# Performance work log

Hardware: AMD Instinct MI355X
Metric: run time of the kernel (lower is better)

Reference implementation:

```python
import jax, jax.numpy as jnp
import numpy as np

N_NODES = 100000
N_EDGES = 3200000
NUM_CLASSES = 10
SQRT3 = 3.0 ** 0.5


def setup_inputs() -> dict:
    key = jax.random.key(0)
    ks = jax.random.split(key, 20)
    f32 = jnp.float32
    return {
        "positions": jax.random.normal(ks[0], (N_NODES, 3), f32) * 5.0,
        "edge_src": jax.random.randint(ks[1], (N_EDGES,), 0, N_NODES, jnp.int32),
        "edge_dst": jax.random.randint(ks[2], (N_EDGES,), 0, N_NODES, jnp.int32),
        # layer1: TP('1x0e', sh) -> '1x0e + 1x1o' -> Linear -> '5x0e + 5x1o'
        "W0_1": jax.random.normal(ks[3], (5, 1), f32),
        "W1_1": jax.random.normal(ks[4], (5, 1, 3), f32),
        "b_1": jax.random.normal(ks[5], (5,), f32),
        # gate1: Linear('5x0e+5x1o' -> '10x0e') uses only the 5 input 0e irreps
        "Wg1": jax.random.normal(ks[6], (10, 5), f32),
        "bg1": jax.random.normal(ks[7], (10,), f32),
        # layer2: TP('5x0e+5x1o', sh) -> 10x0e + 10x1o (+5x1e unused) -> '5x0e+5x1o'
        "W0_2": jax.random.normal(ks[8], (5, 10), f32),
        "W1_2": jax.random.normal(ks[9], (5, 10, 3), f32),
        "b_2": jax.random.normal(ks[10], (5,), f32),
        "Wg2": jax.random.normal(ks[11], (10, 5), f32),
        "bg2": jax.random.normal(ks[12], (10,), f32),
        # layer3: TP -> 10x0e used -> '5x0e'
        "W0_3": jax.random.normal(ks[13], (5, 10), f32),
        "b_3": jax.random.normal(ks[14], (5,), f32),
        "Wg3": jax.random.normal(ks[15], (10, 5), f32),
        "bg3": jax.random.normal(ks[16], (10,), f32),
        "Wout": jax.random.normal(ks[17], (NUM_CLASSES, 5), f32) * 0.3,
        "bout": jax.random.normal(ks[18], (NUM_CLASSES,), f32) * 0.1,
    }


def _sh1(rel):
    # component-normalized real spherical harmonics, lmax=1: Y0 = 1, Y1 = sqrt(3)*r_hat
    r = jnp.linalg.norm(rel, axis=-1, keepdims=True)
    return SQRT3 * rel / jnp.maximum(r, 1e-9)  # [E,3]


def _scatter_mean(x, dst, n):
    s = jax.ops.segment_sum(x, dst, num_segments=n)
    cnt = jax.ops.segment_sum(jnp.ones((x.shape[0],), x.dtype), dst, num_segments=n)
    cnt = jnp.maximum(cnt, 1.0).reshape((n,) + (1,) * (x.ndim - 1))
    return s / cnt


def _layer(s, v, sh1, dst, n, W0, b, W1=None):
    # per-edge CG tensor product of dest-node features with edge SH, then linear, then scatter-mean
    sd = s[dst]                                            # [E,a0] gather 0e feats
    tp_s = [sd]                                            # 0e x 0e(Y0=1) -> 0e
    if v is not None:
        vd = v[dst]                                        # [E,a1,3] gather 1o feats
        tp_s.append(jnp.einsum('eic,ec->ei', vd, sh1) / SQRT3)  # 1o x 1o -> 0e (CG dot)
    tp_s = jnp.concatenate(tp_s, axis=1)
    out_s = _scatter_mean(tp_s @ W0.T + b, dst, n)         # [N,out0]
    if W1 is None:
        return out_s, None
    tp_v = [sd[:, :, None] * sh1[:, None, :]]              # 0e x 1o -> 1o
    if v is not None:
        tp_v.append(vd)                                    # 1o x 0e(Y0=1) -> 1o
    tp_v = jnp.concatenate(tp_v, axis=1)                   # [E,in1,3]
    out_v = _scatter_mean(jnp.einsum('eic,oic->eoc', tp_v, W1), dst, n)
    return out_s, out_v


def _gate(s, v, Wg, bg):
    # ActivationLayer: gate each irrep by GELU of a learned scalar (torch GELU = exact erf)
    g = jax.nn.gelu(s @ Wg.T + bg, approximate=False)
    n0 = s.shape[1]
    gs = g[:, :n0] * s
    if v is None:
        return gs, None
    return gs, g[:, n0:n0 + v.shape[1], None] * v


def reference(positions, edge_src, edge_dst, W0_1, W1_1, b_1, Wg1, bg1,
              W0_2, W1_2, b_2, Wg2, bg2, W0_3, b_3, Wg3, bg3, Wout, bout):
    n = positions.shape[0]
    rel = positions[edge_dst] - positions[edge_src]
    sh1 = _sh1(rel)
    s = jnp.ones((n, 1), positions.dtype)  # dummy '1x0e' starting node features
    s, v = _layer(s, None, sh1, edge_dst, n, W0_1, b_1, W1_1)
    s, v = _gate(s, v, Wg1, bg1)
    s, v = _layer(s, v, sh1, edge_dst, n, W0_2, b_2, W1_2)
    s, v = _gate(s, v, Wg2, bg2)
    s, _ = _layer(s, v, sh1, edge_dst, n, W0_3, b_3, None)
    s, _ = _gate(s, None, Wg3, bg3)
    pooled = jnp.mean(s, axis=0)                       # avg over nodes -> [5]
    return jax.nn.softmax(pooled @ Wout.T + bout)      # [NUM_CLASSES]
```

## Files before the change

### kernel.cpp

```cpp
#include <hip/hip_runtime.h>
#include <math.h>

#define SQRT3F 1.7320508075688772f
#define INV_SQRT3F 0.57735026918962576f
typedef unsigned long long u64;
typedef unsigned int u32;

#define PK_SCALE 1024.0f
#define PK_MASK  0x7FFFFull

#define NPR2   2048
#define NRG2   49
#define REP2   ((size_t)NRG2 * NPR2)
#define EPB    4096
#define NWAVE  8

#define NPR    4096
#define NRANGE 25

__device__ __forceinline__ float gelu_exact(float x) {
    return 0.5f * x * (1.0f + erff(x * 0.70710678118654752f));
}

__device__ __forceinline__ u64 sh_to_w(float rx, float ry, float rz) {
    float rr = sqrtf(rx*rx + ry*ry + rz*rz);
    float inv = (SQRT3F * PK_SCALE) / fmaxf(rr, 1e-9f);
    u32 ax = (u32)__float2int_rn(rx * inv) + 2048u;
    u32 ay = (u32)__float2int_rn(ry * inv) + 2048u;
    u32 az = (u32)__float2int_rn(rz * inv) + 2048u;
    return (u64)ax | ((u64)ay << 19) | ((u64)az << 38) | (1ull << 57);
}

__global__ __launch_bounds__(512) void scatter_pack_kernel(
    const float* __restrict__ pos, float4* __restrict__ pos4,
    const int* __restrict__ src, const int* __restrict__ dst,
    u32* __restrict__ gbuf, u32* __restrict__ cnts, u32* __restrict__ done,
    int E, int N, int P)
{
    const int p = blockIdx.x;
    if (p >= P) {
        int i = (p - P) * 512 + (int)threadIdx.x;
        if (i < N) pos4[i] = make_float4(pos[3*i], pos[3*i+1], pos[3*i+2], 0.f);
        if (p == P && threadIdx.x == 0) *done = 0;
        return;
    }

    __shared__ u32 whist[NWAVE][NRG2];
    __shared__ u32 base[NRG2];
    __shared__ u32 hist[NRG2];
    __shared__ alignas(16) u32 recbuf[EPB];

    const int wid = threadIdx.x >> 6;
    for (int j = threadIdx.x; j < NWAVE * NRG2; j += 512)
        (&whist[0][0])[j] = 0;
    __syncthreads();

    const int start = p * EPB;
    int end = start + EPB;
    if (end > E) end = E;

    int nk = 0;
    int r[8];
    u32 rec[8], rank[8];
    {
        int d[8], s[8];
        int i0 = start + (int)threadIdx.x * 8;
        if (i0 + 8 <= end) {
            int4 da = *reinterpret_cast<const int4*>(dst + i0);
            int4 db = *reinterpret_cast<const int4*>(dst + i0 + 4);
            int4 sa = *reinterpret_cast<const int4*>(src + i0);
            int4 sb = *reinterpret_cast<const int4*>(src + i0 + 4);
            d[0]=da.x; d[1]=da.y; d[2]=da.z; d[3]=da.w;
            d[4]=db.x; d[5]=db.y; d[6]=db.z; d[7]=db.w;
            s[0]=sa.x; s[1]=sa.y; s[2]=sa.z; s[3]=sa.w;
            s[4]=sb.x; s[5]=sb.y; s[6]=sb.z; s[7]=sb.w;
            nk = 8;
        } else if (i0 < end) {
            nk = end - i0;
            for (int k = 0; k < nk; ++k) { d[k] = dst[i0+k]; s[k] = src[i0+k]; }
        }
        for (int k = 0; k < nk; ++k) {
            r[k] = d[k] >> 11;
            rec[k] = ((u32)s[k] << 11) | ((u32)d[k] & 2047u);
        }
    }
    for (int k = 0; k < nk; ++k) rank[k] = atomicAdd(&whist[wid][r[k]], 1u);
    __syncthreads();

    if (threadIdx.x < NRG2) {
        const int rr = threadIdx.x;
        u32 acc = 0;
        #pragma unroll
        for (int w = 0; w < NWAVE; ++w) {
            u32 t = whist[w][rr];
            whist[w][rr] = acc;
            acc += t;
        }
        hist[rr] = acc;
    }
    __syncthreads();

    if (threadIdx.x < 64) {
        int lane = threadIdx.x;
        u32 h = (lane < NRG2) ? hist[lane] : 0;
        u32 v = h;
        #pragma unroll
        for (int off = 1; off < 64; off <<= 1) {
            u32 t = __shfl_up(v, off);
            if (lane >= off) v += t;
        }
        if (lane < NRG2) base[lane] = v - h;
    }
    __syncthreads();

    for (int k = 0; k < nk; ++k)
        recbuf[base[r[k]] + whist[wid][r[k]] + rank[k]] = rec[k];
    __syncthreads();

    const int total = end - start;
    u32* out = gbuf + (size_t)p * EPB;
    const int total4 = total & ~3;
    uint4* out4 = reinterpret_cast<uint4*>(out);
    const uint4* rb4 = reinterpret_cast<const uint4*>(recbuf);
    for (int j = threadIdx.x; j * 4 < total4; j += 512) out4[j] = rb4[j];
    for (int j = total4 + threadIdx.x; j < total; j += 512) out[j] = recbuf[j];
    if (threadIdx.x < NRG2)
        cnts[p * NRG2 + threadIdx.x] = (base[threadIdx.x] << 16) | hist[threadIdx.x];
}

__global__ __launch_bounds__(256, 8) void gather_kernel(
    const float4* __restrict__ pos4,
    const u32* __restrict__ gbuf, const u32* __restrict__ cnts,
    u64* __restrict__ reps, int P, int R2, int N)
{
    __shared__ u64 bins[NPR2];
    __shared__ u32 segn[64];
    const int r  = blockIdx.x % NRG2;
    const int c2 = blockIdx.x / NRG2;
    const int base = r * NPR2;
    const float4* posd = pos4 + base;

    for (int j = threadIdx.x; j < NPR2; j += 256) bins[j] = 0;
    const int nseg = (P - c2 + R2 - 1) / R2;
    for (int t = threadIdx.x; t < nseg; t += 256)
        segn[t] = cnts[(c2 + t * R2) * NRG2 + r];
    __syncthreads();

    const int wid = threadIdx.x >> 6, lane = threadIdx.x & 63;
    for (int sgi = wid; sgi < nseg; sgi += 4) {
        const int p = c2 + sgi * R2;
        const u32 bc = segn[sgi];
        const u32 n = bc & 0xFFFFu;
        const u32* seg = gbuf + (size_t)p * EPB + (bc >> 16);
        for (u32 t = lane; t < n; t += 128) {
            u32 rec0 = seg[t];
            bool h1 = (t + 64) < n;
            u32 rec1 = h1 ? seg[t + 64] : 0;
            u32 j0 = rec0 & 2047u, s0 = rec0 >> 11;
            float4 ps0 = pos4[s0];
            float4 pd0 = posd[j0];
            u32 j1 = rec1 & 2047u, s1 = rec1 >> 11;
            float4 ps1, pd1;
            if (h1) { ps1 = pos4[s1]; pd1 = posd[j1]; }
            atomicAdd(&bins[j0], sh_to_w(pd0.x-ps0.x, pd0.y-ps0.y, pd0.z-ps0.z));
            if (h1)
                atomicAdd(&bins[j1], sh_to_w(pd1.x-ps1.x, pd1.y-ps1.y, pd1.z-ps1.z));
        }
    }
    __syncthreads();

    u64* outp = reps + (size_t)c2 * REP2 + base;
    for (int j = threadIdx.x; j < NPR2; j += 256) outp[j] = bins[j];
}

__global__ __launch_bounds__(256, 4) void edge_bin_kernel(
    const float* __restrict__ pos,
    const int* __restrict__ src,
    const int* __restrict__ dst,
    u64* __restrict__ reps, int E, int span)
{
    __shared__ u64 bins[NPR];
    __shared__ u32 q[4][128];
    const int g = blockIdx.x;
    const int xcd = g & 7;
    const int slot = g >> 3;
    const int c = xcd + 8 * (slot / NRANGE);
    const int r = slot % NRANGE;
    const int base = r * NPR;
    const int lane = threadIdx.x & 63;
    const int wid  = threadIdx.x >> 6;
    const u64 ltmask = (1ull << lane) - 1ull;

    for (int j = threadIdx.x; j < NPR; j += 256) bins[j] = 0;
    __syncthreads();

    const int start = c * span;
    int end = start + span;
    if (end > E) end = E;
    const int niter = (end > start) ? ((end - start + 1023) >> 10) : 0;
    int qcount = 0;

    auto process = [&](u32 i2) {
        int s2 = src[i2]; int d2 = dst[i2];
        u32 j = (u32)(d2 - base);
        atomicAdd(&bins[j], sh_to_w(pos[3*d2+0]-pos[3*s2+0],
                                    pos[3*d2+1]-pos[3*s2+1],
                                    pos[3*d2+2]-pos[3*s2+2]));
    };

    for (int t = 0; t < niter; ++t) {
        int i0 = start + ((int)threadIdx.x << 2) + (t << 10);
        int4 d4 = make_int4(-1, -1, -1, -1);
        if (i0 + 4 <= end) d4 = *reinterpret_cast<const int4*>(dst + i0);
        else if (i0 < end) for (int k = 0; i0 + k < end; ++k) (&d4.x)[k] = dst[i0 + k];
        #pragma unroll
        for (int k = 0; k < 4; ++k) {
            int i = i0 + k;
            bool in = (i < end) && ((u32)((&d4.x)[k] - base) < NPR);
            u64 mask = __ballot(in);
            if (in) q[wid][qcount + __popcll(mask & ltmask)] = (u32)i;
            qcount += (int)__popcll(mask);
            if (qcount >= 64) { qcount -= 64; process(q[wid][qcount + lane]); }
        }
    }
    if (lane < qcount) process(q[wid][lane]);
    __syncthreads();

    u64* outp = reps + (size_t)c * ((size_t)NRANGE * NPR) + base;
    for (int j = threadIdx.x; j < NPR; j += 256) outp[j] = bins[j];
}

template<bool FUSE>
__global__ __launch_bounds__(256) void node_kernel(
    const u64* __restrict__ reps, size_t repStride, int R,
    const float* __restrict__ W0_1, const float* __restrict__ W1_1, const float* __restrict__ b_1,
    const float* __restrict__ Wg1,  const float* __restrict__ bg1,
    const float* __restrict__ W0_2, const float* __restrict__ W1_2, const float* __restrict__ b_2,
    const float* __restrict__ Wg2,  const float* __restrict__ bg2,
    const float* __restrict__ W0_3, const float* __restrict__ b_3,
    const float* __restrict__ Wg3,  const float* __restrict__ bg3,
    float* __restrict__ partials, int N,
    const float* __restrict__ Wout, const float* __restrict__ bout,
    float* __restrict__ out, float invN, u32* __restrict__ done)
{
    int d = blockIdx.x * blockDim.x + threadIdx.x;
    float sf[5] = {0.f, 0.f, 0.f, 0.f, 0.f};

    if (d < N) {
        u64 w = 0;
        int r = 0;
        for (; r + 4 <= R; r += 4) {
            u64 a0 = reps[(size_t)(r+0) * repStride + (u32)d];
            u64 a1 = reps[(size_t)(r+1) * repStride + (u32)d];
            u64 a2 = reps[(size_t)(r+2) * repStride + (u32)d];
            u64 a3 = reps[(size_t)(r+3) * repStride + (u32)d];
            w += a0 + a1 + a2 + a3;
        }
        for (; r < R; ++r) w += reps[(size_t)r * repStride + (u32)d];
        u32 deg = (u32)(w >> 57);
        if (deg > 0) {
            long long bias = (long long)deg << 11;
            float invdS = 1.0f / (PK_SCALE * (float)deg);
            float m[3];
            m[0] = (float)((long long)( w        & PK_MASK) - bias) * invdS;
            m[1] = (float)((long long)((w >> 19) & PK_MASK) - bias) * invdS;
            m[2] = (float)((long long)((w >> 38) & PK_MASK) - bias) * invdS;

            float s1[5], v1[5][3];
            #pragma unroll
            for (int i = 0; i < 5; ++i) {
                s1[i] = W0_1[i] + b_1[i];
                #pragma unroll
                for (int c = 0; c < 3; ++c) v1[i][c] = W1_1[i*3+c] * m[c];
            }
            float g1[10];
            #pragma unroll
            for (int j = 0; j < 10; ++j) {
                float t = bg1[j];
                #pragma unroll
                for (int i = 0; i < 5; ++i) t += Wg1[j*5+i] * s1[i];
                g1[j] = gelu_exact(t);
            }
            #pragma unroll
            for (int i = 0; i < 5; ++i) {
                s1[i] *= g1[i];
                #pragma unroll
                for (int c = 0; c < 3; ++c) v1[i][c] *= g1[5+i];
            }

            float dot1[5];
            #pragma unroll
            for (int i = 0; i < 5; ++i)
                dot1[i] = (v1[i][0]*m[0] + v1[i][1]*m[1] + v1[i][2]*m[2]) * INV_SQRT3F;
            float s2[5];
            #pragma unroll
            for (int o = 0; o < 5; ++o) {
                float t = b_2[o];
                #pragma unroll
                for (int i = 0; i < 5; ++i) t += W0_2[o*10+i] * s1[i];
                #pragma unroll
                for (int i = 0; i < 5; ++i) t += W0_2[o*10+5+i] * dot1[i];
                s2[o] = t;
            }
            float v2[5][3];
            #pragma unroll
            for (int o = 0; o < 5; ++o) {
                #pragma unroll
                for (int c = 0; c < 3; ++c) {
                    float t = 0.f;
                    #pragma unroll
                    for (int i = 0; i < 5; ++i) {
                        t += W1_2[(o*10+i)*3+c]   * (s1[i] * m[c]);
                        t += W1_2[(o*10+5+i)*3+c] * v1[i][c];
                    }
                    v2[o][c] = t;
                }
            }
            float g2[10];
            #pragma unroll
            for (int j = 0; j < 10; ++j) {
                float t = bg2[j];
                #pragma unroll
                for (int i = 0; i < 5; ++i) t += Wg2[j*5+i] * s2[i];
                g2[j] = gelu_exact(t);
            }
            #pragma unroll
            for (int i = 0; i < 5; ++i) {
                s2[i] *= g2[i];
                #pragma unroll
                for (int c = 0; c < 3; ++c) v2[i][c] *= g2[5+i];
            }

            float dot2[5];
            #pragma unroll
            for (int i = 0; i < 5; ++i)
                dot2[i] = (v2[i][0]*m[0] + v2[i][1]*m[1] + v2[i][2]*m[2]) * INV_SQRT3F;
            float s3[5];
            #pragma unroll
            for (int o = 0; o < 5; ++o) {
                float t = b_3[o];
                #pragma unroll
                for (int i = 0; i < 5; ++i) t += W0_3[o*10+i] * s2[i];
                #pragma unroll
                for (int i = 0; i < 5; ++i) t += W0_3[o*10+5+i] * dot2[i];
                s3[o] = t;
            }
            #pragma unroll
            for (int i = 0; i < 5; ++i) {
                float t = bg3[i];
                #pragma unroll
                for (int j = 0; j < 5; ++j) t += Wg3[i*5+j] * s3[j];
                sf[i] = gelu_exact(t) * s3[i];
            }
        }
    }

    #pragma unroll
    for (int k = 0; k < 5; ++k) {
        float v = sf[k];
        for (int off = 32; off > 0; off >>= 1) v += __shfl_down(v, off);
        sf[k] = v;
    }
    __shared__ float lred[4][5];
    __shared__ int islast;
    int wid = threadIdx.x >> 6, lane = threadIdx.x & 63;
    if (lane == 0) {
        #pragma unroll
        for (int k = 0; k < 5; ++k) lred[wid][k] = sf[k];
    }
    __syncthreads();
    if (threadIdx.x == 0) {
        #pragma unroll
        for (int k = 0; k < 5; ++k)
            partials[blockIdx.x * 5 + k] = lred[0][k] + lred[1][k] + lred[2][k] + lred[3][k];
    }

    if (FUSE) {
        if (threadIdx.x == 0) {
            __threadfence();
            u32 old = atomicAdd(done, 1u);
            islast = (old == gridDim.x - 1);
        }
        __syncthreads();
        if (!islast) return;
        __threadfence();
        float s[5] = {0.f, 0.f, 0.f, 0.f, 0.f};
        for (int b = threadIdx.x; b < (int)gridDim.x; b += 256) {
            #pragma unroll
            for (int k = 0; k < 5; ++k) s[k] += partials[b * 5 + k];
        }
        #pragma unroll
        for (int k = 0; k < 5; ++k) {
            float v = s[k];
            for (int off = 32; off > 0; off >>= 1) v += __shfl_down(v, off);
            s[k] = v;
        }
        __syncthreads();
        if (lane == 0) {
            #pragma unroll
            for (int k = 0; k < 5; ++k) lred[wid][k] = s[k];
        }
        __syncthreads();
        if (threadIdx.x == 0) {
            float pooled[5];
            #pragma unroll
            for (int i = 0; i < 5; ++i)
                pooled[i] = (lred[0][i] + lred[1][i] + lred[2][i] + lred[3][i]) * invN;
            float lg[10], mx = -1e30f;
            #pragma unroll
            for (int j = 0; j < 10; ++j) {
                float t = bout[j];
                #pragma unroll
                for (int i = 0; i < 5; ++i) t += Wout[j*5+i] * pooled[i];
                lg[j] = t;
                mx = fmaxf(mx, t);
            }
            float se = 0.f;
            #pragma unroll
            for (int j = 0; j < 10; ++j) { lg[j] = expf(lg[j] - mx); se += lg[j]; }
            float inv = 1.0f / se;
            #pragma unroll
            for (int j = 0; j < 10; ++j) out[j] = lg[j] * inv;
        }
    }
}

__global__ __launch_bounds__(256) void finalize_kernel(
    const float* __restrict__ partials, int nb,
    const float* __restrict__ Wout, const float* __restrict__ bout,
    float* __restrict__ out, float invN)
{
    float s[5] = {0.f, 0.f, 0.f, 0.f, 0.f};
    for (int b = threadIdx.x; b < nb; b += 256) {
        #pragma unroll
        for (int k = 0; k < 5; ++k) s[k] += partials[b * 5 + k];
    }
    #pragma unroll
    for (int k = 0; k < 5; ++k) {
        float v = s[k];
        for (int off = 32; off > 0; off >>= 1) v += __shfl_down(v, off);
        s[k] = v;
    }
    __shared__ float lred[4][5];
    int wid = threadIdx.x >> 6, lane = threadIdx.x & 63;
    if (lane == 0) {
        #pragma unroll
        for (int k = 0; k < 5; ++k) lred[wid][k] = s[k];
    }
    __syncthreads();
    if (threadIdx.x == 0) {
        float pooled[5];
        #pragma unroll
        for (int i = 0; i < 5; ++i)
            pooled[i] = (lred[0][i] + lred[1][i] + lred[2][i] + lred[3][i]) * invN;
        float lg[10], mx = -1e30f;
        #pragma unroll
        for (int j = 0; j < 10; ++j) {
            float t = bout[j];
            #pragma unroll
            for (int i = 0; i < 5; ++i) t += Wout[j*5+i] * pooled[i];
            lg[j] = t;
            mx = fmaxf(mx, t);
        }
        float se = 0.f;
        #pragma unroll
        for (int j = 0; j < 10; ++j) { lg[j] = expf(lg[j] - mx); se += lg[j]; }
        float inv = 1.0f / se;
        #pragma unroll
        for (int j = 0; j < 10; ++j) out[j] = lg[j] * inv;
    }
}

extern "C" void kernel_launch(void* const* d_in, const int* in_sizes, int n_in,
                              void* d_out, int out_size, void* d_ws, size_t ws_size,
                              hipStream_t stream) {
    const float* pos  = (const float*)d_in[0];
    const int*   esrc = (const int*)d_in[1];
    const int*   edst = (const int*)d_in[2];
    const float* W0_1 = (const float*)d_in[3];
    const float* W1_1 = (const float*)d_in[4];
    const float* b_1  = (const float*)d_in[5];
    const float* Wg1  = (const float*)d_in[6];
    const float* bg1  = (const float*)d_in[7];
    const float* W0_2 = (const float*)d_in[8];
    const float* W1_2 = (const float*)d_in[9];
    const float* b_2  = (const float*)d_in[10];
    const float* Wg2  = (const float*)d_in[11];
    const float* bg2  = (const float*)d_in[12];
    const float* W0_3 = (const float*)d_in[13];
    const float* b_3  = (const float*)d_in[14];
    const float* Wg3  = (const float*)d_in[15];
    const float* bg3  = (const float*)d_in[16];
    const float* Wout = (const float*)d_in[17];
    const float* bout = (const float*)d_in[18];

    const int N = in_sizes[0] / 3;
    const int E = in_sizes[1];
    const int nblocks = (N + 255) / 256;
    const int P = (E + EPB - 1) / EPB;
    const int packBlocks = (N + 511) / 512;

    {
        const int r2c[4] = {32, 16, 8, 4};
        for (int a = 0; a < 4; ++a) {
            int R2 = r2c[a];
            size_t off = 16384;
            size_t o_ctr  = off; off += 256;
            size_t o_pos4 = off; off += ((size_t)N * 16 + 255) & ~(size_t)255;
            size_t o_reps = off; off += (size_t)R2 * REP2 * 8;
            size_t o_cnts = off; off += ((size_t)P * NRG2 * 4 + 255) & ~(size_t)255;
            size_t o_gbuf = off; off += (size_t)P * EPB * 4;
            if (off > ws_size) continue;

            float*  partials = (float*)d_ws;
            u32*    done     = (u32*)((char*)d_ws + o_ctr);
            float4* pos4     = (float4*)((char*)d_ws + o_pos4);
            u64*    reps     = (u64*)((char*)d_ws + o_reps);
            u32*    cnts     = (u32*)((char*)d_ws + o_cnts);
            u32*    gbuf     = (u32*)((char*)d_ws + o_gbuf);

            scatter_pack_kernel<<<P + packBlocks, 512, 0, stream>>>(
                pos, pos4, esrc, edst, gbuf, cnts, done, E, N, P);
            gather_kernel<<<NRG2 * R2, 256, 0, stream>>>(pos4, gbuf, cnts,
                reps, P, R2, N);
            node_kernel<true><<<nblocks, 256, 0, stream>>>(reps, REP2, R2,
                W0_1, W1_1, b_1, Wg1, bg1,
                W0_2, W1_2, b_2, Wg2, bg2,
                W0_3, b_3, Wg3, bg3,
                partials, N, Wout, bout, (float*)d_out, 1.0f / (float)N, done);
            return;
        }
    }

    {
        float* partials = (float*)d_ws;
        u64* reps = (u64*)((char*)d_ws + 16384);
        const size_t repStride = (size_t)NRANGE * NPR;
        size_t avail = ws_size > 16384 ? ws_size - 16384 : 0;
        int C = (int)(avail / (repStride * 8));
        if (C > 48) C = 48;
        C &= ~7;
        if (C >= 8) {
            int span = (int)((((size_t)E + C - 1) / C + 3) & ~(size_t)3);
            edge_bin_kernel<<<NRANGE * C, 256, 0, stream>>>(pos, esrc, edst, reps, E, span);
            node_kernel<false><<<nblocks, 256, 0, stream>>>(reps, repStride, C,
                W0_1, W1_1, b_1, Wg1, bg1,
                W0_2, W1_2, b_2, Wg2, bg2,
                W0_3, b_3, Wg3, bg3,
                partials, N, nullptr, nullptr, nullptr, 0.f, nullptr);
            finalize_kernel<<<1, 256, 0, stream>>>(partials, nblocks, Wout, bout,
                                                   (float*)d_out, 1.0f / (float)N);
        }
    }
}
```

Measured before the change: 77.57 us.

## Fuse node math into gather kernel via per-range last-block reduction

The separate node kernel is merged into the gather kernel. Each node range keeps a ticket counter, and the last gather block for that range sums all copies of the replica bins into LDS, runs the per-node network, and writes a per-range partial. A global done counter then lets the final block compute the softmax. This removes one kernel launch and the global re-read of reps by a separate pass, but the node math now runs on only 49 blocks, and the number of replicas drops from 32 to 16, which lowers gather parallelism.

```diff
diff --git a/kernel.cpp b/kernel.cpp
--- a/kernel.cpp
+++ b/kernel.cpp
@@ -31,17 +31,116 @@
     return (u64)ax | ((u64)ay << 19) | ((u64)az << 38) | (1ull << 57);
 }
 
+__device__ void node_math(const float m[3],
+    const float* __restrict__ W0_1, const float* __restrict__ W1_1, const float* __restrict__ b_1,
+    const float* __restrict__ Wg1,  const float* __restrict__ bg1,
+    const float* __restrict__ W0_2, const float* __restrict__ W1_2, const float* __restrict__ b_2,
+    const float* __restrict__ Wg2,  const float* __restrict__ bg2,
+    const float* __restrict__ W0_3, const float* __restrict__ b_3,
+    const float* __restrict__ Wg3,  const float* __restrict__ bg3,
+    float sf[5])
+{
+    float s1[5], v1[5][3];
+    #pragma unroll
+    for (int i = 0; i < 5; ++i) {
+        s1[i] = W0_1[i] + b_1[i];
+        #pragma unroll
+        for (int c = 0; c < 3; ++c) v1[i][c] = W1_1[i*3+c] * m[c];
+    }
+    float g1[10];
+    #pragma unroll
+    for (int j = 0; j < 10; ++j) {
+        float t = bg1[j];
+        #pragma unroll
+        for (int i = 0; i < 5; ++i) t += Wg1[j*5+i] * s1[i];
+        g1[j] = gelu_exact(t);
+    }
+    #pragma unroll
+    for (int i = 0; i < 5; ++i) {
+        s1[i] *= g1[i];
+        #pragma unroll
+        for (int c = 0; c < 3; ++c) v1[i][c] *= g1[5+i];
+    }
+    float dot1[5];
+    #pragma unroll
+    for (int i = 0; i < 5; ++i)
+        dot1[i] = (v1[i][0]*m[0] + v1[i][1]*m[1] + v1[i][2]*m[2]) * INV_SQRT3F;
+    float s2[5];
+    #pragma unroll
+    for (int o = 0; o < 5; ++o) {
+        float t = b_2[o];
+        #pragma unroll
+        for (int i = 0; i < 5; ++i) t += W0_2[o*10+i] * s1[i];
+        #pragma unroll
+        for (int i = 0; i < 5; ++i) t += W0_2[o*10+5+i] * dot1[i];
+        s2[o] = t;
+    }
+    float v2[5][3];
+    #pragma unroll
+    for (int o = 0; o < 5; ++o) {
+        #pragma unroll
+        for (int c = 0; c < 3; ++c) {
+            float t = 0.f;
+            #pragma unroll
+            for (int i = 0; i < 5; ++i) {
+                t += W1_2[(o*10+i)*3+c]   * (s1[i] * m[c]);
+                t += W1_2[(o*10+5+i)*3+c] * v1[i][c];
+            }
+            v2[o][c] = t;
+        }
+    }
+    float g2[10];
+    #pragma unroll
+    for (int j = 0; j < 10; ++j) {
+        float t = bg2[j];
+        #pragma unroll
+        for (int i = 0; i < 5; ++i) t += Wg2[j*5+i] * s2[i];
+        g2[j] = gelu_exact(t);
+    }
+    #pragma unroll
+    for (int i = 0; i < 5; ++i) {
+        s2[i] *= g2[i];
+        #pragma unroll
+        for (int c = 0; c < 3; ++c) v2[i][c] *= g2[5+i];
+    }
+    float dot2[5];
+    #pragma unroll
+    for (int i = 0; i < 5; ++i)
+        dot2[i] = (v2[i][0]*m[0] + v2[i][1]*m[1] + v2[i][2]*m[2]) * INV_SQRT3F;
+    float s3[5];
+    #pragma unroll
+    for (int o = 0; o < 5; ++o) {
+        float t = b_3[o];
+        #pragma unroll
+        for (int i = 0; i < 5; ++i) t += W0_3[o*10+i] * s2[i];
+        #pragma unroll
+        for (int i = 0; i < 5; ++i) t += W0_3[o*10+5+i] * dot2[i];
+        s3[o] = t;
+    }
+    #pragma unroll
+    for (int i = 0; i < 5; ++i) {
+        float t = bg3[i];
+        #pragma unroll
+        for (int j = 0; j < 5; ++j) t += Wg3[i*5+j] * s3[j];
+        sf[i] += gelu_exact(t) * s3[i];
+    }
+}
+
 __global__ __launch_bounds__(512) void scatter_pack_kernel(
     const float* __restrict__ pos, float4* __restrict__ pos4,
     const int* __restrict__ src, const int* __restrict__ dst,
-    u32* __restrict__ gbuf, u32* __restrict__ cnts, u32* __restrict__ done,
+    u32* __restrict__ gbuf, u32* __restrict__ cnts,
+    u32* __restrict__ done, u32* __restrict__ rtick,
     int E, int N, int P)
 {
     const int p = blockIdx.x;
     if (p >= P) {
         int i = (p - P) * 512 + (int)threadIdx.x;
         if (i < N) pos4[i] = make_float4(pos[3*i], pos[3*i+1], pos[3*i+2], 0.f);
-        if (p == P && threadIdx.x == 0) *done = 0;
+        if (p == P && threadIdx.x < 64) {
+            if (threadIdx.x == 0) *done = 0;
+            if (threadIdx.x < NRG2) rtick[threadIdx.x] = 0;
+        }
         return;
     }
 
@@ -128,10 +227,19 @@
         cnts[p * NRG2 + threadIdx.x] = (base[threadIdx.x] << 16) | hist[threadIdx.x];
 }
 
-__global__ __launch_bounds__(256, 8) void gather_kernel(
+__global__ __launch_bounds__(256) void gather_node_kernel(
     const float4* __restrict__ pos4,
     const u32* __restrict__ gbuf, const u32* __restrict__ cnts,
-    u64* __restrict__ reps, int P, int R2, int N)
+    u64* __restrict__ reps, u32* __restrict__ rtick, u32* __restrict__ done,
+    float* __restrict__ partials, int P, int R2, int N,
+    const float* __restrict__ W0_1, const float* __restrict__ W1_1, const float* __restrict__ b_1,
+    const float* __restrict__ Wg1,  const float* __restrict__ bg1,
+    const float* __restrict__ W0_2, const float* __restrict__ W1_2, const float* __restrict__ b_2,
+    const float* __restrict__ Wg2,  const float* __restrict__ bg2,
+    const float* __restrict__ W0_3, const float* __restrict__ b_3,
+    const float* __restrict__ Wg3,  const float* __restrict__ bg3,
+    const float* __restrict__ Wout, const float* __restrict__ bout,
+    float* __restrict__ out, float invN)
 {
     __shared__ u64 bins[NPR2];
     __shared__ u32 segn[64];
@@ -171,6 +279,86 @@
 
     u64* outp = reps + (size_t)c2 * REP2 + base;
     for (int j = threadIdx.x; j < NPR2; j += 256) outp[j] = bins[j];
+
+    __shared__ int lastflag;
+    if (threadIdx.x == 0) {
+        __threadfence();
+        lastflag = (atomicAdd(&rtick[r], 1u) == (u32)(R2 - 1));
+    }
+    __syncthreads();
+    if (!lastflag) return;
+    __threadfence();
+
+    for (int c = 0; c < R2; ++c) {
+        if (c == c2) continue;
+        const u64* sl = reps + (size_t)c * REP2 + base;
+        for (int j = threadIdx.x; j < NPR2; j += 256) bins[j] += sl[j];
+    }
+    __syncthreads();
+
+    float sf[5] = {0.f, 0.f, 0.f, 0.f, 0.f};
+    for (int q = 0; q < NPR2 / 256; ++q) {
+        u64 w = bins[q * 256 + threadIdx.x];
+        u32 deg = (u32)(w >> 57);
+        if (deg > 0) {
+            long long bs = (long long)deg << 11;
+            float invdS = 1.0f / (PK_SCALE * (float)deg);
+            float m[3];
+            m[0] = (float)((long long)( w        & PK_MASK) - bs) * invdS;
+            m[1] = (float)((long long)((w >> 19) & PK_MASK) - bs) * invdS;
+            m[2] = (float)((long long)((w >> 38) & PK_MASK) - bs) * invdS;
+            node_math(m, W0_1, W1_1, b_1, Wg1, bg1, W0_2, W1_2, b_2, Wg2, bg2,
+                      W0_3, b_3, Wg3, bg3, sf);
+        }
+    }
+
+    #pragma unroll
+    for (int k = 0; k < 5; ++k) {
+        float v = sf[k];
+        for (int off = 32; off > 0; off >>= 1) v += __shfl_down(v, off);
+        sf[k] = v;
+    }
+    __shared__ float lred[4][5];
+    if (lane == 0) {
+        #pragma unroll
+        for (int k = 0; k < 5; ++k) lred[wid][k] = sf[k];
+    }
+    __syncthreads();
+    if (threadIdx.x == 0) {
+        #pragma unroll
+        for (int k = 0; k < 5; ++k)
+            partials[r * 5 + k] = lred[0][k] + lred[1][k] + lred[2][k] + lred[3][k];
+        __threadfence();
+        lastflag = (atomicAdd(done, 1u) == NRG2 - 1);
+    }
+    __syncthreads();
+    if (!lastflag) return;
+    __threadfence();
+
+    if (threadIdx.x == 0) {
+        float pooled[5] = {0.f, 0.f, 0.f, 0.f, 0.f};
+        for (int rr = 0; rr < NRG2; ++rr) {
+            #pragma unroll
+            for (int k = 0; k < 5; ++k) pooled[k] += partials[rr * 5 + k];
+        }
+        #pragma unroll
+        for (int k = 0; k < 5; ++k) pooled[k] *= invN;
+        float lg[10], mx = -1e30f;
+        #pragma unroll
+        for (int j = 0; j < 10; ++j) {
+            float t = bout[j];
+            #pragma unroll
+            for (int i = 0; i < 5; ++i) t += Wout[j*5+i] * pooled[i];
+            lg[j] = t;
+            mx = fmaxf(mx, t);
+        }
+        float se = 0.f;
+        #pragma unroll
+        for (int j = 0; j < 10; ++j) { lg[j] = expf(lg[j] - mx); se += lg[j]; }
+        float inv = 1.0f / se;
+        #pragma unroll
+        for (int j = 0; j < 10; ++j) out[j] = lg[j] * inv;
+    }
 }
 
 __global__ __launch_bounds__(256, 4) void edge_bin_kernel(
@@ -230,7 +418,6 @@
     for (int j = threadIdx.x; j < NPR; j += 256) outp[j] = bins[j];
 }
 
-template<bool FUSE>
 __global__ __launch_bounds__(256) void node_kernel(
     const u64* __restrict__ reps, size_t repStride, int R,
     const float* __restrict__ W0_1, const float* __restrict__ W1_1, const float* __restrict__ b_1,
@@ -239,119 +426,24 @@
     const float* __restrict__ Wg2,  const float* __restrict__ bg2,
     const float* __restrict__ W0_3, const float* __restrict__ b_3,
     const float* __restrict__ Wg3,  const float* __restrict__ bg3,
-    float* __restrict__ partials, int N,
-    const float* __restrict__ Wout, const float* __restrict__ bout,
-    float* __restrict__ out, float invN, u32* __restrict__ done)
+    float* __restrict__ partials, int N)
 {
     int d = blockIdx.x * blockDim.x + threadIdx.x;
     float sf[5] = {0.f, 0.f, 0.f, 0.f, 0.f};
 
     if (d < N) {
         u64 w = 0;
-        int r = 0;
-        for (; r + 4 <= R; r += 4) {
-            u64 a0 = reps[(size_t)(r+0) * repStride + (u32)d];
-            u64 a1 = reps[(size_t)(r+1) * repStride + (u32)d];
-            u64 a2 = reps[(size_t)(r+2) * repStride + (u32)d];
-            u64 a3 = reps[(size_t)(r+3) * repStride + (u32)d];
-            w += a0 + a1 + a2 + a3;
-        }
-        for (; r < R; ++r) w += reps[(size_t)r * repStride + (u32)d];
+        for (int r = 0; r < R; ++r) w += reps[(size_t)r * repStride + (u32)d];
         u32 deg = (u32)(w >> 57);
         if (deg > 0) {
-            long long bias = (long long)deg << 11;
+            long long bs = (long long)deg << 11;
             float invdS = 1.0f / (PK_SCALE * (float)deg);
             float m[3];
-            m[0] = (float)((long long)( w        & PK_MASK) - bias) * invdS;
-            m[1] = (float)((long long)((w >> 19) & PK_MASK) - bias) * invdS;
-            m[2] = (float)((long long)((w >> 38) & PK_MASK) - bias) * invdS;
-
-            float s1[5], v1[5][3];
-            #pragma unroll
-            for (int i = 0; i < 5; ++i) {
-                s1[i] = W0_1[i] + b_1[i];
-                #pragma unroll
-                for (int c = 0; c < 3; ++c) v1[i][c] = W1_1[i*3+c] * m[c];
-            }
-            float g1[10];
-            #pragma unroll
-            for (int j = 0; j < 10; ++j) {
-                float t = bg1[j];
-                #pragma unroll
-                for (int i = 0; i < 5; ++i) t += Wg1[j*5+i] * s1[i];
-                g1[j] = gelu_exact(t);
-            }
-            #pragma unroll
-            for (int i = 0; i < 5; ++i) {
-                s1[i] *= g1[i];
-                #pragma unroll
-                for (int c = 0; c < 3; ++c) v1[i][c] *= g1[5+i];
-            }
-
-            float dot1[5];
-            #pragma unroll
-            for (int i = 0; i < 5; ++i)
-                dot1[i] = (v1[i][0]*m[0] + v1[i][1]*m[1] + v1[i][2]*m[2]) * INV_SQRT3F;
-            float s2[5];
-            #pragma unroll
-            for (int o = 0; o < 5; ++o) {
-                float t = b_2[o];
-                #pragma unroll
-                for (int i = 0; i < 5; ++i) t += W0_2[o*10+i] * s1[i];
-                #pragma unroll
-                for (int i = 0; i < 5; ++i) t += W0_2[o*10+5+i] * dot1[i];
-                s2[o] = t;
-            }
-            float v2[5][3];
-            #pragma unroll
-            for (int o = 0; o < 5; ++o) {
-                #pragma unroll
-                for (int c = 0; c < 3; ++c) {
-                    float t = 0.f;
-                    #pragma unroll
-                    for (int i = 0; i < 5; ++i) {
-                        t += W1_2[(o*10+i)*3+c]   * (s1[i] * m[c]);
-                        t += W1_2[(o*10+5+i)*3+c] * v1[i][c];
-                    }
-                    v2[o][c] = t;
-                }
-            }
-            float g2[10];
-            #pragma unroll
-            for (int j = 0; j < 10; ++j) {
-                float t = bg2[j];
-                #pragma unroll
-                for (int i = 0; i < 5; ++i) t += Wg2[j*5+i] * s2[i];
-                g2[j] = gelu_exact(t);
-            }
-            #pragma unroll
-            for (int i = 0; i < 5; ++i) {
-                s2[i] *= g2[i];
-                #pragma unroll
-                for (int c = 0; c < 3; ++c) v2[i][c] *= g2[5+i];
-            }
-
-            float dot2[5];
-            #pragma unroll
-            for (int i = 0; i < 5; ++i)
-                dot2[i] = (v2[i][0]*m[0] + v2[i][1]*m[1] + v2[i][2]*m[2]) * INV_SQRT3F;
-            float s3[5];
-            #pragma unroll
-            for (int o = 0; o < 5; ++o) {
-                float t = b_3[o];
-                #pragma unroll
-                for (int i = 0; i < 5; ++i) t += W0_3[o*10+i] * s2[i];
-                #pragma unroll
-                for (int i = 0; i < 5; ++i) t += W0_3[o*10+5+i] * dot2[i];
-                s3[o] = t;
-            }
-            #pragma unroll
-            for (int i = 0; i < 5; ++i) {
-                float t = bg3[i];
-                #pragma unroll
-                for (int j = 0; j < 5; ++j) t += Wg3[i*5+j] * s3[j];
-                sf[i] = gelu_exact(t) * s3[i];
-            }
+            m[0] = (float)((long long)( w        & PK_MASK) - bs) * invdS;
+            m[1] = (float)((long long)((w >> 19) & PK_MASK) - bs) * invdS;
+            m[2] = (float)((long long)((w >> 38) & PK_MASK) - bs) * invdS;
+            node_math(m, W0_1, W1_1, b_1, Wg1, bg1, W0_2, W1_2, b_2, Wg2, bg2,
+                      W0_3, b_3, Wg3, bg3, sf);
         }
     }
 
@@ -362,7 +454,6 @@
         sf[k] = v;
     }
     __shared__ float lred[4][5];
-    __shared__ int islast;
     int wid = threadIdx.x >> 6, lane = threadIdx.x & 63;
     if (lane == 0) {
         #pragma unroll
@@ -373,55 +464,6 @@
         #pragma unroll
         for (int k = 0; k < 5; ++k)
             partials[blockIdx.x * 5 + k] = lred[0][k] + lred[1][k] + lred[2][k] + lred[3][k];
-    }
-
-    if (FUSE) {
-        if (threadIdx.x == 0) {
-            __threadfence();
-            u32 old = atomicAdd(done, 1u);
-            islast = (old == gridDim.x - 1);
-        }
-        __syncthreads();
-        if (!islast) return;
-        __threadfence();
-        float s[5] = {0.f, 0.f, 0.f, 0.f, 0.f};
-        for (int b = threadIdx.x; b < (int)gridDim.x; b += 256) {
-            #pragma unroll
-            for (int k = 0; k < 5; ++k) s[k] += partials[b * 5 + k];
-        }
-        #pragma unroll
-        for (int k = 0; k < 5; ++k) {
-            float v = s[k];
-            for (int off = 32; off > 0; off >>= 1) v += __shfl_down(v, off);
-            s[k] = v;
-        }
-        __syncthreads();
-        if (lane == 0) {
-            #pragma unroll
-            for (int k = 0; k < 5; ++k) lred[wid][k] = s[k];
-        }
-        __syncthreads();
-        if (threadIdx.x == 0) {
-            float pooled[5];
-            #pragma unroll
-            for (int i = 0; i < 5; ++i)
-                pooled[i] = (lred[0][i] + lred[1][i] + lred[2][i] + lred[3][i]) * invN;
-            float lg[10], mx = -1e30f;
-            #pragma unroll
-            for (int j = 0; j < 10; ++j) {
-                float t = bout[j];
-                #pragma unroll
-                for (int i = 0; i < 5; ++i) t += Wout[j*5+i] * pooled[i];
-                lg[j] = t;
-                mx = fmaxf(mx, t);
-            }
-            float se = 0.f;
-            #pragma unroll
-            for (int j = 0; j < 10; ++j) { lg[j] = expf(lg[j] - mx); se += lg[j]; }
-            float inv = 1.0f / se;
-            #pragma unroll
-            for (int j = 0; j < 10; ++j) out[j] = lg[j] * inv;
-        }
     }
 }
 
@@ -501,11 +543,11 @@
     const int packBlocks = (N + 511) / 512;
 
     {
-        const int r2c[4] = {32, 16, 8, 4};
+        const int r2c[4] = {16, 8, 4, 2};
         for (int a = 0; a < 4; ++a) {
             int R2 = r2c[a];
             size_t off = 16384;
-            size_t o_ctr  = off; off += 256;
+            size_t o_ctr  = off; off += 512;
             size_t o_pos4 = off; off += ((size_t)N * 16 + 255) & ~(size_t)255;
             size_t o_reps = off; off += (size_t)R2 * REP2 * 8;
             size_t o_cnts = off; off += ((size_t)P * NRG2 * 4 + 255) & ~(size_t)255;
@@ -514,20 +556,20 @@
 
             float*  partials = (float*)d_ws;
             u32*    done     = (u32*)((char*)d_ws + o_ctr);
+            u32*    rtick    = (u32*)((char*)d_ws + o_ctr + 64);
             float4* pos4     = (float4*)((char*)d_ws + o_pos4);
             u64*    reps     = (u64*)((char*)d_ws + o_reps);
             u32*    cnts     = (u32*)((char*)d_ws + o_cnts);
             u32*    gbuf     = (u32*)((char*)d_ws + o_gbuf);
 
             scatter_pack_kernel<<<P + packBlocks, 512, 0, stream>>>(
-                pos, pos4, esrc, edst, gbuf, cnts, done, E, N, P);
-            gather_kernel<<<NRG2 * R2, 256, 0, stream>>>(pos4, gbuf, cnts,
-                reps, P, R2, N);
-            node_kernel<true><<<nblocks, 256, 0, stream>>>(reps, REP2, R2,
+                pos, pos4, esrc, edst, gbuf, cnts, done, rtick, E, N, P);
+            gather_node_kernel<<<NRG2 * R2, 256, 0, stream>>>(pos4, gbuf, cnts,
+                reps, rtick, done, partials, P, R2, N,
                 W0_1, W1_1, b_1, Wg1, bg1,
                 W0_2, W1_2, b_2, Wg2, bg2,
                 W0_3, b_3, Wg3, bg3,
-                partials, N, Wout, bout, (float*)d_out, 1.0f / (float)N, done);
+                Wout, bout, (float*)d_out, 1.0f / (float)N);
             return;
         }
     }
@@ -543,11 +585,11 @@
         if (C >= 8) {
             int span = (int)((((size_t)E + C - 1) / C + 3) & ~(size_t)3);
             edge_bin_kernel<<<NRANGE * C, 256, 0, stream>>>(pos, esrc, edst, reps, E, span);
-            node_kernel<false><<<nblocks, 256, 0, stream>>>(reps, repStride, C,
+            node_kernel<<<nblocks, 256, 0, stream>>>(reps, repStride, C,
                 W0_1, W1_1, b_1, Wg1, bg1,
                 W0_2, W1_2, b_2, Wg2, bg2,
                 W0_3, b_3, Wg3, bg3,
-                partials, N, nullptr, nullptr, nullptr, 0.f, nullptr);
+                partials, N);
             finalize_kernel<<<1, 256, 0, stream>>>(partials, nblocks, Wout, bout,
                                                    (float*)d_out, 1.0f / (float)N);
         }
```

Measured after the change: 200.1 us. +157.9%, slower.
